# Kernel optimization log

Measured on AMD Instinct MI355X. Metric: run time of the kernel, lower is better.

## Reference

```python
import jax, jax.numpy as jnp
import numpy as np

B, T, D_IN, D_OUT, H = 2, 2048, 1024, 1024, 16
HD = D_OUT // H


def setup_inputs() -> dict:
    key = jax.random.key(0)
    ks = jax.random.split(key, 6)
    s_in = 1.0 / np.sqrt(D_IN)
    s_out = 1.0 / np.sqrt(D_OUT)
    return {
        "x": jax.random.normal(ks[0], (B, T, D_IN), dtype=jnp.float32),
        # torch nn.Linear stores weight as (out_features, in_features)
        "Wq": jax.random.uniform(ks[1], (D_OUT, D_IN), jnp.float32, -s_in, s_in),
        "Wk": jax.random.uniform(ks[2], (D_OUT, D_IN), jnp.float32, -s_in, s_in),
        "Wv": jax.random.uniform(ks[3], (D_OUT, D_IN), jnp.float32, -s_in, s_in),
        "Wo": jax.random.uniform(ks[4], (D_OUT, D_OUT), jnp.float32, -s_out, s_out),
        "bo": jax.random.uniform(ks[5], (D_OUT,), jnp.float32, -s_out, s_out),
    }


def reference(x, Wq, Wk, Wv, Wo, bo):
    b, t, _ = x.shape
    q = jnp.einsum("btd,ed->bte", x, Wq).reshape(b, t, H, HD).transpose(0, 2, 1, 3)
    k = jnp.einsum("btd,ed->bte", x, Wk).reshape(b, t, H, HD).transpose(0, 2, 1, 3)
    v = jnp.einsum("btd,ed->bte", x, Wv).reshape(b, t, H, HD).transpose(0, 2, 1, 3)
    # [b, h, q, k] materialized scores, masked then scaled (as in source)
    scores = jnp.einsum("bhqd,bhkd->bhqk", q, k)
    causal = jnp.triu(jnp.ones((t, t), dtype=bool), k=1)
    scores = jnp.where(causal, -jnp.inf, scores)
    attn = jax.nn.softmax(scores / jnp.sqrt(jnp.float32(HD)), axis=-1)
    ctx = jnp.einsum("bhqk,bhkd->bhqd", attn, v)
    # NOTE: the source does .view(b, t, d_out) WITHOUT transposing (b,h,t,hd)
    # back to (b,t,h,hd). We replicate that reshape faithfully.
    ctx = ctx.reshape(b, t, D_OUT)
    return jnp.einsum("btd,ed->bte", ctx, Wo) + bo
```

## Files before the change

### kernel.cpp

```cpp
#include <hip/hip_runtime.h>
#include <math.h>

#define BB 2
#define TT 2048
#define DD 1024
#define NH 16
#define HDD 64

typedef __attribute__((ext_vector_type(8))) short v8s;
typedef __attribute__((ext_vector_type(4))) short v4s;
typedef __attribute__((ext_vector_type(4))) float f32x4;

__device__ __forceinline__ unsigned short f2bf(float f) {
    union { float f; unsigned int u; } c; c.f = f;
    unsigned int r = c.u + 0x7FFF + ((c.u >> 16) & 1);
    return (unsigned short)(r >> 16);
}

__device__ __forceinline__ void gload_lds16(const void* g, void* l) {
    __builtin_amdgcn_global_load_lds(
        (const __attribute__((address_space(1))) void*)g,
        (__attribute__((address_space(3))) void*)l, 16, 0, 0);
}

__device__ __forceinline__ f32x4 mfma16x16x16bf16(v4s a, v4s b, f32x4 c) {
#if __has_builtin(__builtin_amdgcn_mfma_f32_16x16x16bf16_1k)
    return __builtin_amdgcn_mfma_f32_16x16x16bf16_1k(a, b, c, 0, 0, 0);
#else
    f32x4 d;
    asm("v_mfma_f32_16x16x16_bf16 %0, %1, %2, %0"
        : "=v"(d) : "v"(a), "v"(b), "0"(c));
    return d;
#endif
}

__global__ __launch_bounds__(256) void cast5_kernel(
    const float* __restrict__ x, const float* __restrict__ wq,
    const float* __restrict__ wk, const float* __restrict__ wv,
    const float* __restrict__ wo,
    unsigned short* __restrict__ xo, unsigned short* __restrict__ wqo,
    unsigned short* __restrict__ wko, unsigned short* __restrict__ wvo,
    unsigned short* __restrict__ woo)
{
    const float* s; unsigned short* d; int n4;
    switch (blockIdx.y) {
        case 0: s = x;  d = xo;  n4 = BB * TT * DD / 4; break;
        case 1: s = wq; d = wqo; n4 = DD * DD / 4; break;
        case 2: s = wk; d = wko; n4 = DD * DD / 4; break;
        case 3: s = wv; d = wvo; n4 = DD * DD / 4; break;
        default: s = wo; d = woo; n4 = DD * DD / 4; break;
    }
    int i = blockIdx.x * 256 + threadIdx.x;
    if (i < n4) {
        float4 v = ((const float4*)s)[i];
        ushort4 o;
        o.x = f2bf(v.x); o.y = f2bf(v.y); o.z = f2bf(v.z); o.w = f2bf(v.w);
        ((ushort4*)d)[i] = o;
    }
}

__global__ __launch_bounds__(256) void qkv_mfma(
    const unsigned short* __restrict__ x,
    const unsigned short* __restrict__ wq, const unsigned short* __restrict__ wk,
    const unsigned short* __restrict__ wv,
    unsigned short* __restrict__ qo, unsigned short* __restrict__ ko,
    unsigned short* __restrict__ vo)
{
    __shared__ unsigned short SMEM[16384];

    const int tid = threadIdx.x;
    const int lane = tid & 63;
    const int wid = tid >> 6;
    const int l15 = lane & 15, quad = lane >> 4;

    const int m0 = blockIdx.x << 7;
    const int ny = blockIdx.y;
    const int which = ny >> 3;
    const int n0 = (ny & 7) << 7;
    const unsigned short* W = (which == 0) ? wq : (which == 1) ? wk : wv;

    const int wm = (wid >> 1) << 6;
    const int wn = (wid & 1) << 6;

    const int f0 = (wid << 11) + (lane << 4);
    const int row0 = f0 >> 6, cs0 = (f0 & 63) >> 1;
    const int f1 = f0 + 1024;
    const int row1 = f1 >> 6, cs1 = (f1 & 63) >> 1;

    char* const smem = (char*)SMEM;

#define QKV_STAGE(k0, buf)                                                     \
    do {                                                                       \
        gload_lds16(&x[(size_t)(m0 + row0) * DD + (k0) + cs0],                 \
                    smem + (buf) * 8192 + f0);                                 \
        gload_lds16(&x[(size_t)(m0 + row1) * DD + (k0) + cs1],                 \
                    smem + (buf) * 8192 + f1);                                 \
        gload_lds16(&W[(size_t)(n0 + row0) * DD + (k0) + cs0],                 \
                    smem + 16384 + (buf) * 8192 + f0);                         \
        gload_lds16(&W[(size_t)(n0 + row1) * DD + (k0) + cs1],                 \
                    smem + 16384 + (buf) * 8192 + f1);                         \
    } while (0)

    f32x4 acc[4][4] = {};

    QKV_STAGE(0, 0);
    __syncthreads();

    int cur = 0;
    for (int k0 = 0; k0 < DD; k0 += 32) {
        if (k0 + 32 < DD) QKV_STAGE(k0 + 32, cur ^ 1);

        const char* Ab = smem + cur * 8192;
        const char* Bb = smem + 16384 + cur * 8192;
        v8s af[4], bf[4];
#pragma unroll
        for (int i = 0; i < 4; ++i)
            af[i] = *(const v8s*)(Ab + (wm + (i << 4) + l15) * 64 + (quad << 4));
#pragma unroll
        for (int j = 0; j < 4; ++j)
            bf[j] = *(const v8s*)(Bb + (wn + (j << 4) + l15) * 64 + (quad << 4));
#pragma unroll
        for (int i = 0; i < 4; ++i)
#pragma unroll
            for (int j = 0; j < 4; ++j)
                acc[i][j] = __builtin_amdgcn_mfma_f32_16x16x32_bf16(af[i], bf[j], acc[i][j], 0, 0, 0);

        __syncthreads();
        cur ^= 1;
    }
#undef QKV_STAGE

    if (which == 2) {
#pragma unroll
        for (int i = 0; i < 4; ++i)
#pragma unroll
            for (int j = 0; j < 4; ++j) {
                const int n = n0 + wn + (j << 4) + l15;
                const int h = n >> 6, hd = n & 63;
                const int mb = m0 + wm + (i << 4) + (quad << 2);
                const int b = mb >> 11, t = mb & 2047;
                ushort4 pk;
                pk.x = f2bf(acc[i][j][0]); pk.y = f2bf(acc[i][j][1]);
                pk.z = f2bf(acc[i][j][2]); pk.w = f2bf(acc[i][j][3]);
                *(ushort4*)&vo[((((size_t)(b * NH + h) << 6) + hd) << 11) + t] = pk;
            }
    } else {
        unsigned short* outp = (which == 0) ? qo : ko;
        const float sc = (which == 1) ? 0.125f : 1.0f;
#pragma unroll
        for (int p = 0; p < 2; ++p) {
            __syncthreads();
            if ((wid >> 1) == p) {
#pragma unroll
                for (int i = 0; i < 4; ++i)
#pragma unroll
                    for (int j = 0; j < 4; ++j)
#pragma unroll
                        for (int r = 0; r < 4; ++r) {
                            const int row = (i << 4) + (quad << 2) + r;
                            SMEM[row * 136 + wn + (j << 4) + l15] = f2bf(acc[i][j][r] * sc);
                        }
            }
            __syncthreads();
            const int rr = tid >> 2;
            const int cg = (tid & 3) << 5;
            const int m = m0 + (p << 6) + rr;
            const int b = m >> 11, t = m & 2047;
#pragma unroll
            for (int k2 = 0; k2 < 4; ++k2) {
                const int n = n0 + cg + (k2 << 3);
                const int h = n >> 6, hd = n & 63;
                const uint4 val = *(const uint4*)&SMEM[rr * 136 + cg + (k2 << 3)];
                *(uint4*)&outp[(((size_t)(b * NH + h) * TT + t) << 6) + hd] = val;
            }
        }
    }
}

__global__ __launch_bounds__(256) void attn_mfma(
    const unsigned short* __restrict__ q, const unsigned short* __restrict__ k,
    const unsigned short* __restrict__ vt, unsigned short* __restrict__ ctx)
{
    __shared__ unsigned short Qs[64][72];
    __shared__ unsigned short Ks[64][72];
    __shared__ unsigned short Vts[64][72];

    const int tid = threadIdx.x;
    const int lane = tid & 63;
    const int wid = tid >> 6;
    const int l15 = lane & 15, quad = lane >> 4;
    const int bh = blockIdx.y;

    const unsigned short* qb = q + (size_t)bh * TT * HDD;
    const unsigned short* kb = k + (size_t)bh * TT * HDD;
    const unsigned short* vb = vt + (size_t)bh * HDD * TT;
    unsigned short* cb = ctx + (size_t)bh * TT * HDD;

    const int cr = tid >> 3;
    const int cc = (tid & 7) << 3;

    for (int half = 0; half < 2; ++half) {
        const int qt = half ? (31 - (int)blockIdx.x) : (int)blockIdx.x;
        const int q0 = qt << 6;
        const int qrow = q0 + (wid << 4) + l15;

        __syncthreads();
#pragma unroll
        for (int u = 0; u < 2; ++u) {
            const int r = cr + (u << 5);
            *(uint4*)&Qs[r][cc] = *(const uint4*)&qb[(size_t)(q0 + r) * HDD + cc];
        }
        __syncthreads();

        v8s qf[2];
#pragma unroll
        for (int c = 0; c < 2; ++c)
            qf[c] = *(const v8s*)&Qs[(wid << 4) + l15][(c << 5) + (quad << 3)];

        float m_i = -INFINITY, l_i = 0.f;
        f32x4 o[4] = {};

        for (int jt = 0; jt <= qt; ++jt) {
            const int k0 = jt << 6;
            __syncthreads();
#pragma unroll
            for (int u = 0; u < 2; ++u) {
                const int r = cr + (u << 5);
                *(uint4*)&Ks[r][cc] = *(const uint4*)&kb[(size_t)(k0 + r) * HDD + cc];
                *(uint4*)&Vts[r][cc] = *(const uint4*)&vb[((size_t)r << 11) + k0 + cc];
            }
            __syncthreads();

            f32x4 s[4] = {};
#pragma unroll
            for (int m = 0; m < 4; ++m) {
                const v8s kf0 = *(const v8s*)&Ks[(m << 4) + l15][quad << 3];
                const v8s kf1 = *(const v8s*)&Ks[(m << 4) + l15][32 + (quad << 3)];
                s[m] = __builtin_amdgcn_mfma_f32_16x16x32_bf16(kf0, qf[0], s[m], 0, 0, 0);
                s[m] = __builtin_amdgcn_mfma_f32_16x16x32_bf16(kf1, qf[1], s[m], 0, 0, 0);
            }

            if (jt == qt) {
#pragma unroll
                for (int m = 0; m < 4; ++m) {
                    const int kc = k0 + (m << 4) + (quad << 2);
#pragma unroll
                    for (int r = 0; r < 4; ++r)
                        if (kc + r > qrow) s[m][r] = -INFINITY;
                }
            }

            float mx = fmaxf(fmaxf(s[0][0], s[0][1]), fmaxf(s[0][2], s[0][3]));
            mx = fmaxf(mx, fmaxf(fmaxf(s[1][0], s[1][1]), fmaxf(s[1][2], s[1][3])));
            mx = fmaxf(mx, fmaxf(fmaxf(s[2][0], s[2][1]), fmaxf(s[2][2], s[2][3])));
            mx = fmaxf(mx, fmaxf(fmaxf(s[3][0], s[3][1]), fmaxf(s[3][2], s[3][3])));
            mx = fmaxf(mx, __shfl_xor(mx, 16));
            mx = fmaxf(mx, __shfl_xor(mx, 32));
            const float m_new = fmaxf(m_i, mx);
            const float alpha = __expf(m_i - m_new);
            m_i = m_new;

            float sum = 0.f;
            v4s pf[4];
#pragma unroll
            for (int m = 0; m < 4; ++m) {
                v4s t;
#pragma unroll
                for (int r = 0; r < 4; ++r) {
                    const float pv = __expf(s[m][r] - m_new);
                    sum += pv;
                    t[r] = (short)f2bf(pv);
                }
                pf[m] = t;
            }
            sum += __shfl_xor(sum, 16);
            sum += __shfl_xor(sum, 32);
            l_i = l_i * alpha + sum;

#pragma unroll
            for (int m = 0; m < 4; ++m)
#pragma unroll
                for (int r = 0; r < 4; ++r)
                    o[m][r] *= alpha;

#pragma unroll
            for (int m = 0; m < 4; ++m)
#pragma unroll
                for (int c = 0; c < 4; ++c) {
                    const v4s vf = *(const v4s*)&Vts[(m << 4) + l15][(c << 4) + (quad << 2)];
                    o[m] = mfma16x16x16bf16(vf, pf[c], o[m]);
                }
        }

        const float linv = 1.f / l_i;
#pragma unroll
        for (int m = 0; m < 4; ++m) {
            ushort4 st;
            st.x = f2bf(o[m][0] * linv); st.y = f2bf(o[m][1] * linv);
            st.z = f2bf(o[m][2] * linv); st.w = f2bf(o[m][3] * linv);
            *(ushort4*)&cb[((size_t)qrow << 6) + (m << 4) + (quad << 2)] = st;
        }
    }
}

__global__ __launch_bounds__(256) void oproj_mfma(
    const unsigned short* __restrict__ c, const unsigned short* __restrict__ wo,
    const float* __restrict__ bo, float* __restrict__ out)
{
    __shared__ unsigned short SMEM[16384];

    const int tid = threadIdx.x;
    const int lane = tid & 63;
    const int wid = tid >> 6;
    const int l15 = lane & 15, quad = lane >> 4;

    const int m0 = blockIdx.x << 7;
    const int n0 = blockIdx.y << 7;
    const int wm = (wid >> 1) << 6, wn = (wid & 1) << 6;

    const int f0 = (wid << 11) + (lane << 4);
    const int row0 = f0 >> 6, cs0 = (f0 & 63) >> 1;
    const int f1 = f0 + 1024;
    const int row1 = f1 >> 6, cs1 = (f1 & 63) >> 1;

    char* const smem = (char*)SMEM;

#define OP_STAGE(k0, buf)                                                      \
    do {                                                                       \
        gload_lds16(&c[(size_t)(m0 + row0) * DD + (k0) + cs0],                 \
                    smem + (buf) * 8192 + f0);                                 \
        gload_lds16(&c[(size_t)(m0 + row1) * DD + (k0) + cs1],                 \
                    smem + (buf) * 8192 + f1);                                 \
        gload_lds16(&wo[(size_t)(n0 + row0) * DD + (k0) + cs0],                \
                    smem + 16384 + (buf) * 8192 + f0);                         \
        gload_lds16(&wo[(size_t)(n0 + row1) * DD + (k0) + cs1],                \
                    smem + 16384 + (buf) * 8192 + f1);                         \
    } while (0)

    f32x4 acc[4][4] = {};

    OP_STAGE(0, 0);
    __syncthreads();

    int cur = 0;
    for (int k0 = 0; k0 < DD; k0 += 32) {
        if (k0 + 32 < DD) OP_STAGE(k0 + 32, cur ^ 1);

        const char* Ab = smem + cur * 8192;
        const char* Bb = smem + 16384 + cur * 8192;
        v8s af[4], bf[4];
#pragma unroll
        for (int i = 0; i < 4; ++i)
            af[i] = *(const v8s*)(Ab + (wm + (i << 4) + l15) * 64 + (quad << 4));
#pragma unroll
        for (int j = 0; j < 4; ++j)
            bf[j] = *(const v8s*)(Bb + (wn + (j << 4) + l15) * 64 + (quad << 4));
#pragma unroll
        for (int i = 0; i < 4; ++i)
#pragma unroll
            for (int j = 0; j < 4; ++j)
                acc[i][j] = __builtin_amdgcn_mfma_f32_16x16x32_bf16(af[i], bf[j], acc[i][j], 0, 0, 0);

        __syncthreads();
        cur ^= 1;
    }
#undef OP_STAGE

#pragma unroll
    for (int j = 0; j < 4; ++j) {
        const int n = n0 + wn + (j << 4) + l15;
        const float bias = bo[n];
#pragma unroll
        for (int i = 0; i < 4; ++i) {
            const int mb = m0 + wm + (i << 4) + (quad << 2);
#pragma unroll
            for (int r = 0; r < 4; ++r)
                out[(size_t)(mb + r) * DD + n] = acc[i][j][r] + bias;
        }
    }
}

extern "C" void kernel_launch(void* const* d_in, const int* in_sizes, int n_in,
                              void* d_out, int out_size, void* d_ws, size_t ws_size,
                              hipStream_t stream) {
    const float* x  = (const float*)d_in[0];
    const float* Wq = (const float*)d_in[1];
    const float* Wk = (const float*)d_in[2];
    const float* Wv = (const float*)d_in[3];
    const float* Wo = (const float*)d_in[4];
    const float* bo = (const float*)d_in[5];
    float* out = (float*)d_out;

    const size_t NX = (size_t)BB * TT * DD;
    const size_t NW = (size_t)DD * DD;

    unsigned short* xb  = (unsigned short*)d_ws;
    unsigned short* wqb = xb + NX;
    unsigned short* wkb = wqb + NW;
    unsigned short* wvb = wkb + NW;
    unsigned short* wob = wvb + NW;
    unsigned short* qb  = wob + NW;
    unsigned short* kb  = qb + NX;
    unsigned short* vtb = kb + NX;
    unsigned short* cbuf = vtb + NX;

    cast5_kernel<<<dim3(4096, 5), 256, 0, stream>>>(x, Wq, Wk, Wv, Wo,
                                                    xb, wqb, wkb, wvb, wob);
    qkv_mfma<<<dim3(32, 24), 256, 0, stream>>>(xb, wqb, wkb, wvb, qb, kb, vtb);
    attn_mfma<<<dim3(16, 32), 256, 0, stream>>>(qb, kb, vtb, cbuf);
    oproj_mfma<<<dim3(32, 8), 256, 0, stream>>>(cbuf, wob, bo, out);
}
```

Measured before the change: 196.4 us.

## Double-buffer K/V tiles in attention with register prefetch and remap block order

Result: faster. 190.3 us (-3.1%).

```diff
diff --git a/kernel.cpp b/kernel.cpp
--- a/kernel.cpp
+++ b/kernel.cpp
@@ -182,14 +182,17 @@
     const unsigned short* __restrict__ vt, unsigned short* __restrict__ ctx)
 {
     __shared__ unsigned short Qs[64][72];
-    __shared__ unsigned short Ks[64][72];
-    __shared__ unsigned short Vts[64][72];
+    __shared__ unsigned short Ks[2][64][72];
+    __shared__ unsigned short Vts[2][64][72];
 
     const int tid = threadIdx.x;
     const int lane = tid & 63;
     const int wid = tid >> 6;
     const int l15 = lane & 15, quad = lane >> 4;
-    const int bh = blockIdx.y;
+
+    const int lin = (int)blockIdx.x + ((int)blockIdx.y << 4);
+    const int bh = lin & 31;
+    const int pair = lin >> 5;
 
     const unsigned short* qb = q + (size_t)bh * TT * HDD;
     const unsigned short* kb = k + (size_t)bh * TT * HDD;
@@ -200,7 +203,7 @@
     const int cc = (tid & 7) << 3;
 
     for (int half = 0; half < 2; ++half) {
-        const int qt = half ? (31 - (int)blockIdx.x) : (int)blockIdx.x;
+        const int qt = half ? (31 - pair) : pair;
         const int q0 = qt << 6;
         const int qrow = q0 + (wid << 4) + l15;
 
@@ -210,6 +213,16 @@
             const int r = cr + (u << 5);
             *(uint4*)&Qs[r][cc] = *(const uint4*)&qb[(size_t)(q0 + r) * HDD + cc];
         }
+        {
+            uint4 k0r = *(const uint4*)&kb[(size_t)cr * HDD + cc];
+            uint4 k1r = *(const uint4*)&kb[(size_t)(cr + 32) * HDD + cc];
+            uint4 v0r = *(const uint4*)&vb[((size_t)cr << 11) + cc];
+            uint4 v1r = *(const uint4*)&vb[((size_t)(cr + 32) << 11) + cc];
+            *(uint4*)&Ks[0][cr][cc] = k0r;
+            *(uint4*)&Ks[0][cr + 32][cc] = k1r;
+            *(uint4*)&Vts[0][cr][cc] = v0r;
+            *(uint4*)&Vts[0][cr + 32][cc] = v1r;
+        }
         __syncthreads();
 
         v8s qf[2];
@@ -221,21 +234,25 @@
         f32x4 o[4] = {};
 
         for (int jt = 0; jt <= qt; ++jt) {
+            const int cur = jt & 1;
+
+            uint4 k0r, k1r, v0r, v1r;
+            const bool pre = (jt < qt);
+            if (pre) {
+                const int kn = (jt + 1) << 6;
+                k0r = *(const uint4*)&kb[(size_t)(kn + cr) * HDD + cc];
+                k1r = *(const uint4*)&kb[(size_t)(kn + cr + 32) * HDD + cc];
+                v0r = *(const uint4*)&vb[((size_t)cr << 11) + kn + cc];
+                v1r = *(const uint4*)&vb[((size_t)(cr + 32) << 11) + kn + cc];
+            }
+
             const int k0 = jt << 6;
-            __syncthreads();
-#pragma unroll
-            for (int u = 0; u < 2; ++u) {
-                const int r = cr + (u << 5);
-                *(uint4*)&Ks[r][cc] = *(const uint4*)&kb[(size_t)(k0 + r) * HDD + cc];
-                *(uint4*)&Vts[r][cc] = *(const uint4*)&vb[((size_t)r << 11) + k0 + cc];
-            }
-            __syncthreads();
 
             f32x4 s[4] = {};
 #pragma unroll
             for (int m = 0; m < 4; ++m) {
-                const v8s kf0 = *(const v8s*)&Ks[(m << 4) + l15][quad << 3];
-                const v8s kf1 = *(const v8s*)&Ks[(m << 4) + l15][32 + (quad << 3)];
+                const v8s kf0 = *(const v8s*)&Ks[cur][(m << 4) + l15][quad << 3];
+                const v8s kf1 = *(const v8s*)&Ks[cur][(m << 4) + l15][32 + (quad << 3)];
                 s[m] = __builtin_amdgcn_mfma_f32_16x16x32_bf16(kf0, qf[0], s[m], 0, 0, 0);
                 s[m] = __builtin_amdgcn_mfma_f32_16x16x32_bf16(kf1, qf[1], s[m], 0, 0, 0);
             }
@@ -287,9 +304,18 @@
             for (int m = 0; m < 4; ++m)
 #pragma unroll
                 for (int c = 0; c < 4; ++c) {
-                    const v4s vf = *(const v4s*)&Vts[(m << 4) + l15][(c << 4) + (quad << 2)];
+                    const v4s vf = *(const v4s*)&Vts[cur][(m << 4) + l15][(c << 4) + (quad << 2)];
                     o[m] = mfma16x16x16bf16(vf, pf[c], o[m]);
                 }
+
+            if (pre) {
+                const int nxt = cur ^ 1;
+                *(uint4*)&Ks[nxt][cr][cc] = k0r;
+                *(uint4*)&Ks[nxt][cr + 32][cc] = k1r;
+                *(uint4*)&Vts[nxt][cr][cc] = v0r;
+                *(uint4*)&Vts[nxt][cr + 32][cc] = v1r;
+            }
+            __syncthreads();
         }
 
         const float linv = 1.f / l_i;
```
